# Kernel tuning notes

Hardware: AMD Instinct MI355X
Metric: run time of the kernel (lower is better)

Reference implementation:

```python
import jax, jax.numpy as jnp
import numpy as np

B, S, H, L, NH, DH, FF = 64, 256, 768, 12, 12, 64, 3072
V, MAXP, NTYPE, NI, NS = 30522, 512, 2, 10, 64


def setup_inputs() -> dict:
    key = jax.random.key(0)
    ks = iter(jax.random.split(key, 40))
    n = lambda shp, s=0.02: jax.random.normal(next(ks), shp, jnp.float32) * s
    inp = {
        'input_ids': jax.random.randint(next(ks), (B, S), 0, V),
        'attention_mask': jnp.ones((B, S), jnp.int32),
        'token_type_ids': jnp.zeros((B, S), jnp.int32),
        'intent_labels': jax.random.randint(next(ks), (B,), 0, NI),
        'slot_labels': jax.random.randint(next(ks), (B, S), 0, NS),
        'word_emb': n((V, H)), 'pos_emb': n((MAXP, H)), 'type_emb': n((NTYPE, H)),
        'emb_ln_g': jnp.ones((H,)), 'emb_ln_b': jnp.zeros((H,)),
        'Wq': n((L, H, H)), 'bq': jnp.zeros((L, H)),
        'Wk': n((L, H, H)), 'bk': jnp.zeros((L, H)),
        'Wv': n((L, H, H)), 'bv': jnp.zeros((L, H)),
        'Wo': n((L, H, H)), 'bo': jnp.zeros((L, H)),
        'ln1_g': jnp.ones((L, H)), 'ln1_b': jnp.zeros((L, H)),
        'W1': n((L, H, FF)), 'b1': jnp.zeros((L, FF)),
        'W2': n((L, FF, H)), 'b2': jnp.zeros((L, H)),
        'ln2_g': jnp.ones((L, H)), 'ln2_b': jnp.zeros((L, H)),
        'Wi': n((H, NI)), 'bi': jnp.zeros((NI,)),
        'Ws': n((H, NS)), 'bs': jnp.zeros((NS,)),
        'crf_start': n((NS,), 0.1), 'crf_end': n((NS,), 0.1),
        'crf_trans': n((NS, NS), 0.1),
    }
    return inp


def _ln(x, g, b):
    m = x.mean(-1, keepdims=True)
    v = jnp.square(x - m).mean(-1, keepdims=True)
    return (x - m) * jax.lax.rsqrt(v + 1e-12) * g + b


def _forward(params, input_ids, attention_mask, token_type_ids, intent_labels, slot_labels):
    (word_emb, pos_emb, type_emb, emb_ln_g, emb_ln_b,
     Wq, bq, Wk, bk, Wv, bv, Wo, bo, ln1_g, ln1_b,
     W1, b1, W2, b2, ln2_g, ln2_b,
     Wi, bi, Ws, bs, crf_start, crf_end, crf_trans) = params
    Bn, Sn = input_ids.shape
    Hn = word_emb.shape[1]
    dh = Hn // NH
    # BERT embeddings (dropout is identity in eval)
    x = word_emb[input_ids] + pos_emb[:Sn][None] + type_emb[token_type_ids]
    x = _ln(x, emb_ln_g, emb_ln_b)
    bias = (1.0 - attention_mask.astype(x.dtype))[:, None, None, :] * -1e9  # [B,1,1,S]

    def layer(h, p):
        wq, cq, wk, ck, wv, cv, wo, co, g1, d1, w1, e1, w2, e2, g2, d2 = p
        q = (h @ wq + cq).reshape(Bn, Sn, NH, dh)
        k = (h @ wk + ck).reshape(Bn, Sn, NH, dh)
        v = (h @ wv + cv).reshape(Bn, Sn, NH, dh)
        sc = jnp.einsum('bqnd,bknd->bnqk', q, k) / jnp.sqrt(jnp.float32(dh)) + bias
        a = jax.nn.softmax(sc, axis=-1)
        ctx = jnp.einsum('bnqk,bknd->bqnd', a, v).reshape(Bn, Sn, Hn)
        h2 = _ln(h + ctx @ wo + co, g1, d1)
        ff = jax.nn.gelu(h2 @ w1 + e1, approximate=False)
        return _ln(h2 + ff @ w2 + e2, g2, d2), None

    x, _ = jax.lax.scan(layer, x, (Wq, bq, Wk, bk, Wv, bv, Wo, bo,
                                   ln1_g, ln1_b, W1, b1, W2, b2, ln2_g, ln2_b))
    intent_logits = x[:, 0, :] @ Wi + bi           # [B, NI]
    slot_logits = x @ Ws + bs                      # [B, S, NS]
    # intent cross-entropy (mean over batch)
    lp = jax.nn.log_softmax(intent_logits, axis=-1)
    intent_loss = -jnp.take_along_axis(lp, intent_labels[:, None], axis=1).mean()
    # CRF log-likelihood
    mask = attention_mask.astype(slot_logits.dtype)
    em, tags = slot_logits, slot_labels
    t0 = tags[:, 0]
    score = crf_start[t0] + jnp.take_along_axis(em[:, 0, :], t0[:, None], axis=1)[:, 0]
    prev, cur = tags[:, :-1], tags[:, 1:]
    step_sc = crf_trans[prev, cur] + jnp.take_along_axis(em[:, 1:, :], cur[..., None], axis=2)[..., 0]
    score = score + (step_sc * mask[:, 1:]).sum(1)
    lengths = attention_mask.sum(1)
    last_tag = jnp.take_along_axis(tags, (lengths - 1)[:, None].astype(tags.dtype), axis=1)[:, 0]
    score = score + crf_end[last_tag]
    em_t = jnp.swapaxes(em, 0, 1)    # [S,B,C]
    mk_t = jnp.swapaxes(mask, 0, 1)  # [S,B]
    alpha0 = crf_start[None, :] + em_t[0]

    def crf_step(alpha, xs):
        e, m = xs
        nxt = jax.scipy.special.logsumexp(alpha[:, :, None] + crf_trans[None], axis=1) + e
        return jnp.where(m[:, None] > 0, nxt, alpha), None

    alpha, _ = jax.lax.scan(crf_step, alpha0, (em_t[1:], mk_t[1:]))
    logZ = jax.scipy.special.logsumexp(alpha + crf_end[None, :], axis=1)
    llh = score - logZ                # per-sequence log-likelihood
    crf_loss = -llh.mean()
    return intent_loss + 2.0 * crf_loss


def reference(input_ids, attention_mask, token_type_ids, intent_labels, slot_labels,
              word_emb, pos_emb, type_emb, emb_ln_g, emb_ln_b,
              Wq, bq, Wk, bk, Wv, bv, Wo, bo, ln1_g, ln1_b,
              W1, b1, W2, b2, ln2_g, ln2_b,
              Wi, bi, Ws, bs, crf_start, crf_end, crf_trans):
    params = (word_emb, pos_emb, type_emb, emb_ln_g, emb_ln_b,
              Wq, bq, Wk, bk, Wv, bv, Wo, bo, ln1_g, ln1_b,
              W1, b1, W2, b2, ln2_g, ln2_b,
              Wi, bi, Ws, bs, crf_start, crf_end, crf_trans)
    return _forward(params, input_ids, attention_mask, token_type_ids, intent_labels, slot_labels)
```

## Files before the change

kernel.cpp:

```cpp
#include <hip/hip_runtime.h>
#include <stdint.h>

typedef unsigned short u16;
typedef __attribute__((ext_vector_type(8))) short bh8;
typedef __attribute__((ext_vector_type(4))) float f4;

#define DEV static __device__ __forceinline__

DEV u16 f2bf(float f){ union{float f; uint32_t u;} v; v.f=f; uint32_t r=v.u + 0x7FFFu + ((v.u>>16)&1u); return (u16)(r>>16); }
DEV float bf2f(u16 u){ union{uint32_t u; float f;} v; v.u=((uint32_t)u)<<16; return v.f; }

DEV void mfma16(f4& d, bh8 a, bh8 b){
  d = __builtin_amdgcn_mfma_f32_16x16x32_bf16(a, b, d, 0, 0, 0);
}

DEV float gelu(float v){
  float x = v*0.70710678118f;
  float ax = fabsf(x);
  float tt = 1.0f/(1.0f + 0.3275911f*ax);
  float y = 1.0f - (((((1.061405429f*tt - 1.453152027f)*tt) + 1.421413741f)*tt
                     - 0.284496736f)*tt + 0.254829592f)*tt*__expf(-ax*ax);
  float e = (x<0.f)? -y : y;
  return 0.5f*v*(1.0f+e);
}

#define GLD16(g,l) __builtin_amdgcn_global_load_lds( \
    (__attribute__((address_space(1))) void*)(void*)(g), \
    (__attribute__((address_space(3))) void*)(void*)(l), 16, 0, 0)

struct GemmP { const u16* A; const u16* B; int K; void* C; int ldc;
               const float* b0; const float* b1; const float* b2; const u16* res; };

template<int EPI>
DEV void epi_store(const GemmP& p, int gr, int gc, float v){
  if(EPI==0){
    const float* bp = (gc<768)? p.b0 : (gc<1536? p.b1 : p.b2);
    const int bc = (gc<768)? gc : (gc<1536? gc-768 : gc-1536);
    ((u16*)p.C)[(size_t)gr*p.ldc + gc] = f2bf(v + bp[bc]);
  } else if(EPI==1){
    v += p.b0[gc] + bf2f(p.res[(size_t)gr*p.ldc + gc]);
    ((u16*)p.C)[(size_t)gr*p.ldc + gc] = f2bf(v);
  } else if(EPI==2){
    ((u16*)p.C)[(size_t)gr*p.ldc + gc] = f2bf(gelu(v + p.b0[gc]));
  } else {
    v += (gc<64)? p.b0[gc] : 0.f;
    ((float*)p.C)[(size_t)gr*p.ldc + gc] = v;
  }
}

template<int EPI>
__global__ __launch_bounds__(512)
void gemm256(GemmP p){
  extern __shared__ char smem[];
  const int t=threadIdx.x, l=t&63, w=t>>6;
  const int wr=w>>2, wc=w&3;
  const int m0=blockIdx.x*256, n0=blockIdx.y*256;
  const int K=p.K, NT=K>>6;
  const int fl=l&15, fh=l>>4;

  const int r0=(w*1024+l*16)>>7;
  const int cs=(((l&7)^(l>>3))<<4);
  const char* gA0 = (const char*)p.A + ((size_t)(m0+r0)*K)*2 + cs;
  const char* gB0 = (const char*)p.B + ((size_t)(n0+r0)*K)*2 + cs;
  const size_t rowblk = (size_t)64*K*2;
  char* dA = smem + w*1024;
  char* dB = smem + 32768 + w*1024;

  #define SG_A(T,h,buf) do{ const char* _s=gA0 + (size_t)(T)*128 + (size_t)(h)*2*rowblk; \
    char* _d=dA+(buf)*65536+(h)*16384; GLD16(_s,_d); GLD16(_s+rowblk,_d+8192); }while(0)
  #define SG_B(T,h,buf) do{ const char* _s=gB0 + (size_t)(T)*128 + (size_t)(h)*2*rowblk; \
    char* _d=dB+(buf)*65536+(h)*16384; GLD16(_s,_d); GLD16(_s+rowblk,_d+8192); }while(0)

  int oB[4][2], oA[8][2];
#pragma unroll
  for(int nf=0;nf<4;nf++){ const int rw=wc*64+nf*16+fl;
#pragma unroll
    for(int ks=0;ks<2;ks++) oB[nf][ks] = 32768 + rw*128 + ((ks*64+fh*16) ^ ((rw&7)<<4)); }
#pragma unroll
  for(int mf=0;mf<8;mf++){ const int rw=wr*128+mf*16+fl;
#pragma unroll
    for(int ks=0;ks<2;ks++) oA[mf][ks] = rw*128 + ((ks*64+fh*16) ^ ((rw&7)<<4)); }

  f4 acc[8][4] = {};
  bh8 bfA[4][2], bfB[4][2], afA[2][2], afB[2][2];

  #define MFMA_Q(q, AF, BF) do{ \
    __builtin_amdgcn_s_setprio(1); \
    _Pragma("unroll") \
    for(int j=0;j<2;j++) \
      _Pragma("unroll") \
      for(int nf=0;nf<4;nf++){ mfma16(acc[2*(q)+j][nf], AF[j][0], BF[nf][0]); \
                               mfma16(acc[2*(q)+j][nf], AF[j][1], BF[nf][1]); } \
    __builtin_amdgcn_s_setprio(0); }while(0)

  #define WAIT_LGKM do{ asm volatile("s_waitcnt lgkmcnt(0)":::"memory"); \
    __builtin_amdgcn_sched_barrier(0); }while(0)

  #define TILE(T, CUR, BF) do{ \
    const char* sb = smem + ((CUR)<<16); \
     \
    if((T)+1<NT){ SG_A((T)+1,0,(CUR)^1); SG_A((T)+1,1,(CUR)^1); } \
    _Pragma("unroll") \
    for(int nf=0;nf<4;nf++){ BF[nf][0]=*(const bh8*)(sb+oB[nf][0]); BF[nf][1]=*(const bh8*)(sb+oB[nf][1]); } \
    afA[0][0]=*(const bh8*)(sb+oA[0][0]); afA[0][1]=*(const bh8*)(sb+oA[0][1]); \
    afA[1][0]=*(const bh8*)(sb+oA[1][0]); afA[1][1]=*(const bh8*)(sb+oA[1][1]); \
    __builtin_amdgcn_s_barrier(); WAIT_LGKM; \
    MFMA_Q(0, afA, BF); \
    __builtin_amdgcn_s_barrier(); \
     \
    if((T)+2<NT) SG_B((T)+2,0,(CUR)); \
    afB[0][0]=*(const bh8*)(sb+oA[2][0]); afB[0][1]=*(const bh8*)(sb+oA[2][1]); \
    afB[1][0]=*(const bh8*)(sb+oA[3][0]); afB[1][1]=*(const bh8*)(sb+oA[3][1]); \
    __builtin_amdgcn_s_barrier(); WAIT_LGKM; \
    MFMA_Q(1, afB, BF); \
    __builtin_amdgcn_s_barrier(); \
     \
    if((T)+2<NT) SG_B((T)+2,1,(CUR)); \
    afA[0][0]=*(const bh8*)(sb+oA[4][0]); afA[0][1]=*(const bh8*)(sb+oA[4][1]); \
    afA[1][0]=*(const bh8*)(sb+oA[5][0]); afA[1][1]=*(const bh8*)(sb+oA[5][1]); \
    __builtin_amdgcn_s_barrier(); WAIT_LGKM; \
    MFMA_Q(2, afA, BF); \
    __builtin_amdgcn_s_barrier(); \
     \
    afB[0][0]=*(const bh8*)(sb+oA[6][0]); afB[0][1]=*(const bh8*)(sb+oA[6][1]); \
    afB[1][0]=*(const bh8*)(sb+oA[7][0]); afB[1][1]=*(const bh8*)(sb+oA[7][1]); \
    __builtin_amdgcn_s_barrier(); WAIT_LGKM; \
    MFMA_Q(3, afB, BF); \
    if((T)+2<NT)      asm volatile("s_waitcnt vmcnt(4)":::"memory"); \
    else if((T)+1<NT) asm volatile("s_waitcnt vmcnt(0)":::"memory"); \
    __builtin_amdgcn_s_barrier(); \
  }while(0)

  SG_A(0,0,0); SG_A(0,1,0); SG_B(0,0,0); SG_B(0,1,0);
  if(NT>1){ SG_B(1,0,1); SG_B(1,1,1);
            asm volatile("s_waitcnt vmcnt(4)":::"memory"); }
  else    { asm volatile("s_waitcnt vmcnt(0)":::"memory"); }
  __builtin_amdgcn_s_barrier();

  for(int T=0; T<NT; T+=2){
    TILE(T,   0, bfA);
    TILE(T+1, 1, bfB);
  }
  #undef TILE
  #undef SG_A
  #undef SG_B
  #undef MFMA_Q
  #undef WAIT_LGKM

  const int lr=fh*4;
#pragma unroll
  for(int m=0;m<8;m++)
#pragma unroll
  for(int n=0;n<4;n++)
#pragma unroll
  for(int r=0;r<4;r++){
    epi_store<EPI>(p, m0 + wr*128 + m*16 + lr + r, n0 + wc*64 + n*16 + fl, acc[m][n][r]);
  }
}

template<int EPI>
__global__ __launch_bounds__(256)
void gemm_bt(GemmP p){
  __shared__ __align__(16) u16 As[128*32];
  __shared__ __align__(16) u16 Bs[128*32];
  const int t=threadIdx.x, l=t&63, w=t>>6, wr=w>>1, wc=w&1;
  const int fl=l&15, fh=l>>4;
  const int m0=blockIdx.x*128, n0=blockIdx.y*128;
  const int K=p.K, NT=K>>5;
  const int srow=t>>2;
  const int cs=(((t&3) ^ (srow&3))<<4);
  const char* gA = (const char*)p.A + ((size_t)(m0+srow)*K)*2 + cs;
  const char* gB = (const char*)p.B + ((size_t)(n0+srow)*K)*2 + cs;
  const size_t r64 = (size_t)64*K*2;
  char* dA = (char*)As + t*16;
  char* dB = (char*)Bs + t*16;

  int oA2[4], oB2[4];
#pragma unroll
  for(int mf=0;mf<4;mf++){ const int rw=wr*64+mf*16+fl;
    oA2[mf] = rw*64 + ((fh ^ (rw&3))<<4); }
#pragma unroll
  for(int nf=0;nf<4;nf++){ const int rw=wc*64+nf*16+fl;
    oB2[nf] = rw*64 + ((fh ^ (rw&3))<<4); }

  f4 acc[4][4] = {};
  for(int T=0; T<NT; ++T){
    GLD16(gA + (size_t)T*64, dA);
    GLD16(gA + (size_t)T*64 + r64, dA + 4096);
    GLD16(gB + (size_t)T*64, dB);
    GLD16(gB + (size_t)T*64 + r64, dB + 4096);
    __syncthreads();
    bh8 af[4], bfr[4];
#pragma unroll
    for(int mf=0;mf<4;mf++) af[mf]=*(const bh8*)((const char*)As+oA2[mf]);
#pragma unroll
    for(int nf=0;nf<4;nf++) bfr[nf]=*(const bh8*)((const char*)Bs+oB2[nf]);
#pragma unroll
    for(int m=0;m<4;m++)
#pragma unroll
      for(int n=0;n<4;n++) mfma16(acc[m][n], af[m], bfr[n]);
    __syncthreads();
  }
  const int lr=fh*4;
#pragma unroll
  for(int m=0;m<4;m++)
#pragma unroll
  for(int n=0;n<4;n++)
#pragma unroll
  for(int r=0;r<4;r++){
    epi_store<EPI>(p, m0 + wr*64 + m*16 + lr + r, n0 + wc*64 + n*16 + fl, acc[m][n][r]);
  }
}

__global__ __launch_bounds__(256)
void attn_kernel(const u16* __restrict__ qkv, const int* __restrict__ amask, u16* __restrict__ ctx){
  __shared__ __align__(16) u16 Ks[256*64];
  __shared__ __align__(16) u16 Vt[64*256];
  __shared__ __align__(16) u16 Ps[4*64*64];
  __shared__ float biasS[256];
  const int t=threadIdx.x, l=t&63, w=t>>6;
  const int b=blockIdx.x/12, h=blockIdx.x%12;
  biasS[t] = (1.f - (float)amask[b*256+t]) * -1e9f;
  const u16* kb = qkv + ((size_t)b*256)*2304 + 768 + h*64;
  const u16* vb = kb + 768;
#pragma unroll
  for(int i=0;i<8;i++){
    const int c = t + i*256;
    const int row = c>>3, seg = c&7;
    uint4 kv = *(const uint4*)(kb + (size_t)row*2304 + seg*8);
    const int ba = row*128 + seg*16;
    *(uint4*)((char*)Ks + (ba ^ ((row&7)<<4))) = kv;
    uint4 vv = *(const uint4*)(vb + (size_t)row*2304 + seg*8);
    const u16* pv = (const u16*)&vv;
#pragma unroll
    for(int j=0;j<8;j++){
      const int d = seg*8+j;
      const int bb = d*512 + row*2;
      *(u16*)((char*)Vt + (bb ^ ((d&7)<<4))) = pv[j];
    }
  }
  bh8 aq[4][2];
  const u16* qb = qkv + ((size_t)b*256 + w*64)*2304 + h*64;
#pragma unroll
  for(int m=0;m<4;m++)
#pragma unroll
    for(int ks=0;ks<2;ks++)
      aq[m][ks] = *(const bh8*)(qb + (size_t)(m*16+(l&15))*2304 + ks*32 + (l>>4)*8);
  __syncthreads();
  float mrun[4][4], lrun[4][4];
  f4 o[4][4] = {};
#pragma unroll
  for(int m=0;m<4;m++)
#pragma unroll
    for(int r=0;r<4;r++){ mrun[m][r] = -3e38f; lrun[m][r]=0.f; }
  u16* Pw = Ps + w*4096;
  for(int kt=0;kt<4;kt++){
    f4 sacc[4][4] = {};
#pragma unroll
    for(int ks=0;ks<2;ks++)
#pragma unroll
      for(int n=0;n<4;n++){
        const int row = kt*64 + n*16 + (l&15);
        const int by = row*128 + ks*64 + (l>>4)*16;
        bh8 bk = *(const bh8*)((const char*)Ks + (by ^ ((row&7)<<4)));
#pragma unroll
        for(int m=0;m<4;m++) mfma16(sacc[m][n], aq[m][ks], bk);
      }
#pragma unroll
    for(int m=0;m<4;m++){
      float rmax[4] = {-3e38f,-3e38f,-3e38f,-3e38f};
#pragma unroll
      for(int n=0;n<4;n++){
        const float bi = biasS[kt*64 + n*16 + (l&15)];
#pragma unroll
        for(int r=0;r<4;r++){
          float sv = sacc[m][n][r]*0.125f + bi;
          sacc[m][n][r] = sv;
          rmax[r] = fmaxf(rmax[r], sv);
        }
      }
#pragma unroll
      for(int dd=1; dd<16; dd<<=1)
#pragma unroll
        for(int r=0;r<4;r++) rmax[r] = fmaxf(rmax[r], __shfl_xor(rmax[r], dd));
      float psum[4];
#pragma unroll
      for(int r=0;r<4;r++){
        const float mn = fmaxf(mrun[m][r], rmax[r]);
        const float corr = __expf(mrun[m][r] - mn);
        mrun[m][r] = mn;
        lrun[m][r] *= corr;
#pragma unroll
        for(int nd=0; nd<4; nd++) o[m][nd][r] *= corr;
        psum[r] = 0.f;
      }
#pragma unroll
      for(int n=0;n<4;n++)
#pragma unroll
        for(int r=0;r<4;r++){
          const float pvv = __expf(sacc[m][n][r] - mrun[m][r]);
          sacc[m][n][r] = pvv;
          psum[r] += pvv;
        }
#pragma unroll
      for(int dd=1; dd<16; dd<<=1)
#pragma unroll
        for(int r=0;r<4;r++) psum[r] += __shfl_xor(psum[r], dd);
#pragma unroll
      for(int r=0;r<4;r++) lrun[m][r] += psum[r];
#pragma unroll
      for(int n=0;n<4;n++)
#pragma unroll
        for(int r=0;r<4;r++){
          const int prow = m*16 + (l>>4)*4 + r;
          const int pcol = n*16 + (l&15);
          const int by = prow*128 + pcol*2;
          *(u16*)((char*)Pw + (by ^ ((prow&7)<<4))) = f2bf(sacc[m][n][r]);
        }
    }
#pragma unroll
    for(int ks=0;ks<2;ks++){
      bh8 ap[4];
#pragma unroll
      for(int m=0;m<4;m++){
        const int prow = m*16 + (l&15);
        const int by = prow*128 + (ks*32 + (l>>4)*8)*2;
        ap[m] = *(const bh8*)((const char*)Pw + (by ^ ((prow&7)<<4)));
      }
#pragma unroll
      for(int nd=0; nd<4; nd++){
        const int dR = nd*16 + (l&15);
        const int by = dR*512 + (kt*64 + ks*32 + (l>>4)*8)*2;
        bh8 bv = *(const bh8*)((const char*)Vt + (by ^ ((dR&7)<<4)));
#pragma unroll
        for(int m=0;m<4;m++) mfma16(o[m][nd], ap[m], bv);
      }
    }
  }
#pragma unroll
  for(int m=0;m<4;m++)
#pragma unroll
  for(int nd=0; nd<4; nd++)
#pragma unroll
  for(int r=0;r<4;r++){
    const int row = w*64 + m*16 + (l>>4)*4 + r;
    const float vv = o[m][nd][r] / lrun[m][r];
    ctx[((size_t)b*256 + row)*768 + h*64 + nd*16 + (l&15)] = f2bf(vv);
  }
}

__global__ void ln_kernel(const u16* __restrict__ in, const float* __restrict__ g,
                          const float* __restrict__ b, u16* __restrict__ out){
  const int row = blockIdx.x, t = threadIdx.x;
  __shared__ float red[8];
  const u16* rp = in + (size_t)row*768;
  float v[3]; float s=0.f, q=0.f;
#pragma unroll
  for(int i=0;i<3;i++){ float x = bf2f(rp[t + i*256]); v[i]=x; s+=x; q+=x*x; }
#pragma unroll
  for(int dd=1; dd<64; dd<<=1){ s += __shfl_xor(s,dd); q += __shfl_xor(q,dd); }
  if((t&63)==0){ red[t>>6]=s; red[4+(t>>6)]=q; }
  __syncthreads();
  s = red[0]+red[1]+red[2]+red[3];
  q = red[4]+red[5]+red[6]+red[7];
  const float mean = s*(1.f/768.f);
  float var = q*(1.f/768.f) - mean*mean; var = fmaxf(var, 0.f);
  const float rs = rsqrtf(var + 1e-12f);
  u16* op = out + (size_t)row*768;
#pragma unroll
  for(int i=0;i<3;i++){ const int hh=t+i*256; op[hh] = f2bf((v[i]-mean)*rs*g[hh] + b[hh]); }
}

__global__ void embed_ln(const int* __restrict__ ids, const int* __restrict__ tti,
    const float* __restrict__ we, const float* __restrict__ pe, const float* __restrict__ te,
    const float* __restrict__ g, const float* __restrict__ bb, u16* __restrict__ x){
  const int tok = blockIdx.x, t = threadIdx.x;
  __shared__ float red[8];
  const int id = ids[tok], tyid = tti[tok], s0 = tok & 255;
  float v[3]; float s=0.f,q=0.f;
#pragma unroll
  for(int i=0;i<3;i++){
    const int hh = t+i*256;
    float x0 = we[(size_t)id*768+hh] + pe[(size_t)s0*768+hh] + te[(size_t)tyid*768+hh];
    v[i]=x0; s+=x0; q+=x0*x0;
  }
#pragma unroll
  for(int dd=1; dd<64; dd<<=1){ s += __shfl_xor(s,dd); q += __shfl_xor(q,dd); }
  if((t&63)==0){ red[t>>6]=s; red[4+(t>>6)]=q; }
  __syncthreads();
  s = red[0]+red[1]+red[2]+red[3];
  q = red[4]+red[5]+red[6]+red[7];
  const float mean = s*(1.f/768.f);
  float var = q*(1.f/768.f) - mean*mean; var = fmaxf(var, 0.f);
  const float rs = rsqrtf(var + 1e-12f);
#pragma unroll
  for(int i=0;i<3;i++){ const int hh=t+i*256; x[(size_t)tok*768+hh] = f2bf((v[i]-mean)*rs*g[hh] + bb[hh]); }
}

__global__ void transpose_cvt(const float* __restrict__ src, u16* __restrict__ dst, int R, int C){
  __shared__ float sm[32][33];
  const int ntc = C>>5;
  const int tr = blockIdx.x/ntc, tc = blockIdx.x - tr*ntc;
  const int r0 = tr<<5, c0 = tc<<5;
  const int tx = threadIdx.x, ty2 = threadIdx.y;
#pragma unroll
  for(int i=0;i<4;i++) sm[ty2+i*8][tx] = src[(size_t)(r0+ty2+i*8)*C + c0+tx];
  __syncthreads();
#pragma unroll
  for(int i=0;i<4;i++) dst[(size_t)(c0+ty2+i*8)*R + r0+tx] = f2bf(sm[tx][ty2+i*8]);
}

__global__ void conv_layer(const float* __restrict__ Wq, const float* __restrict__ Wk,
    const float* __restrict__ Wv, const float* __restrict__ Wo,
    const float* __restrict__ W1, const float* __restrict__ W2, u16* __restrict__ Wt){
  __shared__ float sm[32][33];
  const int bid = blockIdx.x;
  const float* src; u16* dst; int R, C, tt;
  if(bid<2304){
    R=768; C=768; const int mi = bid/576; tt = bid - mi*576;
    src = (mi==0?Wq: mi==1?Wk: mi==2?Wv: Wo);
    dst = Wt + (size_t)mi*589824;
  } else if(bid<4608){ R=768; C=3072; tt=bid-2304; src=W1; dst=Wt+2359296; }
  else { R=3072; C=768; tt=bid-4608; src=W2; dst=Wt+4718592; }
  const int ntc=C>>5; const int tr=tt/ntc, tc=tt-tr*ntc;
  const int r0=tr<<5, c0=tc<<5, tx=threadIdx.x, ty2=threadIdx.y;
#pragma unroll
  for(int i=0;i<4;i++) sm[ty2+i*8][tx] = src[(size_t)(r0+ty2+i*8)*C + c0+tx];
  __syncthreads();
#pragma unroll
  for(int i=0;i<4;i++) dst[(size_t)(c0+ty2+i*8)*R + r0+tx] = f2bf(sm[tx][ty2+i*8]);
}

__global__ void intent_kernel(const u16* __restrict__ x, const float* __restrict__ Wi,
    const float* __restrict__ bi, const int* __restrict__ lab, float* __restrict__ parts){
  const int b = blockIdx.x, t = threadIdx.x;
  __shared__ float xs[768];
  __shared__ float lg[10];
  const u16* rp = x + ((size_t)b*256)*768;
#pragma unroll
  for(int i=0;i<3;i++) xs[t+i*256] = bf2f(rp[t+i*256]);
  __syncthreads();
  if(t<10){
    float s = bi[t];
    for(int k=0;k<768;k++) s += xs[k]*Wi[(size_t)k*10 + t];
    lg[t] = s;
  }
  __syncthreads();
  if(t==0){
    float m = lg[0];
    for(int j=1;j<10;j++) m = fmaxf(m, lg[j]);
    float se = 0.f;
    for(int j=0;j<10;j++) se += expf(lg[j]-m);
    parts[b] = (logf(se) + m) - lg[lab[b]];
  }
}

__global__ __launch_bounds__(64)
void crf_kernel(const float* __restrict__ em, const int* __restrict__ tags,
    const int* __restrict__ amask, const float* __restrict__ cs, const float* __restrict__ ce,
    const float* __restrict__ tr, float* __restrict__ parts){
  const int b = blockIdx.x, j = threadIdx.x;
  const float* eb = em + (size_t)b*256*128;
  const int* tg = tags + b*256;
  const int* mk = amask + b*256;
  __shared__ __align__(16) float aS[64];
  float Etr[64];
#pragma unroll
  for(int i=0;i<64;i++) Etr[i] = __expf(tr[i*64 + j]);
  float sc = 0.f; int len = 0;
  for(int s=j+1; s<256; s+=64){
    const int pv = tg[s-1], cu = tg[s];
    sc += (tr[pv*64+cu] + eb[(size_t)s*128+cu]) * (float)mk[s];
  }
  for(int s=j; s<256; s+=64) len += mk[s];
#pragma unroll
  for(int dd=1; dd<64; dd<<=1){ sc += __shfl_xor(sc,dd); len += __shfl_xor(len,dd); }
  const int t0 = tg[0];
  float score = sc + cs[t0] + eb[t0] + ce[tg[len-1]];
  float a = __expf(cs[j] + eb[j]);
  float logc = 0.f;
  float em_s = eb[128 + j];
  int   mk_s = mk[1];
  for(int s=1; s<256; s++){
    const int sn = (s<255)? s+1 : s;
    const float em_n = eb[(size_t)sn*128 + j];
    const int   mk_n = mk[sn];
    aS[j] = a;
    __syncthreads();
    float acc0=0.f, acc1=0.f, acc2=0.f, acc3=0.f;
    const float4* ap = (const float4*)aS;
#pragma unroll
    for(int q2=0;q2<16;q2++){
      const float4 av = ap[q2];
      acc0 += av.x*Etr[4*q2+0];
      acc1 += av.y*Etr[4*q2+1];
      acc2 += av.z*Etr[4*q2+2];
      acc3 += av.w*Etr[4*q2+3];
    }
    __syncthreads();
    const float nxt = ((acc0+acc1)+(acc2+acc3)) * __expf(em_s);
    a = (mk_s > 0) ? nxt : a;
    if((s&7)==7){
      const float c = __shfl(a, 0);
      logc += __logf(c);
      a *= (1.f/c);
    }
    em_s = em_n; mk_s = mk_n;
  }
  float v2 = logf(a) + logc + ce[j];
  float am2 = v2;
#pragma unroll
  for(int dd=1; dd<64; dd<<=1) am2 = fmaxf(am2, __shfl_xor(am2,dd));
  float se = __expf(v2 - am2);
#pragma unroll
  for(int dd=1; dd<64; dd<<=1) se += __shfl_xor(se,dd);
  if(j==0) parts[64+b] = (logf(se)+am2) - score;
}

__global__ void final_reduce(const float* __restrict__ parts, float* __restrict__ out){
  const int t = threadIdx.x;
  float a = parts[t], c = parts[64+t];
#pragma unroll
  for(int dd=1; dd<64; dd<<=1){ a += __shfl_xor(a,dd); c += __shfl_xor(c,dd); }
  if(t==0) out[0] = a*(1.f/64.f) + 2.f*c*(1.f/64.f);
}

extern "C" void kernel_launch(void* const* d_in, const int* in_sizes, int n_in,
                              void* d_out, int out_size, void* d_ws, size_t ws_size,
                              hipStream_t stream){
  (void)in_sizes; (void)n_in; (void)out_size;
  const int* ids   = (const int*)d_in[0];
  const int* amask = (const int*)d_in[1];
  const int* tti   = (const int*)d_in[2];
  const int* ilab  = (const int*)d_in[3];
  const int* slab  = (const int*)d_in[4];
  const float* we  = (const float*)d_in[5];
  const float* pe  = (const float*)d_in[6];
  const float* te  = (const float*)d_in[7];
  const float* eg  = (const float*)d_in[8];
  const float* ebt = (const float*)d_in[9];
  const float* Wq  = (const float*)d_in[10];
  const float* bq  = (const float*)d_in[11];
  const float* Wk  = (const float*)d_in[12];
  const float* bkk = (const float*)d_in[13];
  const float* Wv  = (const float*)d_in[14];
  const float* bvv = (const float*)d_in[15];
  const float* Wo  = (const float*)d_in[16];
  const float* bo  = (const float*)d_in[17];
  const float* l1g = (const float*)d_in[18];
  const float* l1b = (const float*)d_in[19];
  const float* W1  = (const float*)d_in[20];
  const float* b1  = (const float*)d_in[21];
  const float* W2  = (const float*)d_in[22];
  const float* b2  = (const float*)d_in[23];
  const float* l2g = (const float*)d_in[24];
  const float* l2b = (const float*)d_in[25];
  const float* Wi  = (const float*)d_in[26];
  const float* bi  = (const float*)d_in[27];
  const float* Wsp = (const float*)d_in[28];
  const float* bs  = (const float*)d_in[29];
  const float* cs  = (const float*)d_in[30];
  const float* ce  = (const float*)d_in[31];
  const float* ctr = (const float*)d_in[32];

  char* ws = (char*)d_ws;
  size_t off = 0;
  auto alloc = [&](size_t bytes)->void*{ void* p = ws + off; off += (bytes+255)&~(size_t)255; return p; };
  u16* x     = (u16*)alloc(16384ull*768*2);
  u16* h2    = (u16*)alloc(16384ull*768*2);
  u16* y     = (u16*)alloc(16384ull*768*2);
  u16* qkv   = (u16*)alloc(16384ull*2304*2);
  u16* cf    = (u16*)alloc(16384ull*3072*2);
  u16* Wt    = (u16*)alloc(7077888ull*2);
  u16* WsT   = (u16*)alloc(128ull*768*2);
  float* slots = (float*)alloc(16384ull*128*4);
  float* parts = (float*)alloc(512);
  if(off > ws_size) return;

  (void)hipFuncSetAttribute((const void*)gemm256<0>, hipFuncAttributeMaxDynamicSharedMemorySize, 131072);
  (void)hipFuncSetAttribute((const void*)gemm256<1>, hipFuncAttributeMaxDynamicSharedMemorySize, 131072);
  (void)hipFuncSetAttribute((const void*)gemm256<2>, hipFuncAttributeMaxDynamicSharedMemorySize, 131072);

  dim3 T256(256), T512(512), T328(32,8);
  embed_ln<<<dim3(16384), T256, 0, stream>>>(ids, tti, we, pe, te, eg, ebt, x);
  transpose_cvt<<<dim3(48), T328, 0, stream>>>(Wsp, WsT, 768, 64);
  for(int L=0; L<12; L++){
    const size_t oH = (size_t)L*768*768, oF = (size_t)L*768*3072;
    conv_layer<<<dim3(6912), T328, 0, stream>>>(Wq+oH, Wk+oH, Wv+oH, Wo+oH, W1+oF, W2+oF, Wt);
    GemmP pq{ x, Wt, 768, qkv, 2304, bq+L*768, bkk+L*768, bvv+L*768, nullptr };
    gemm256<0><<<dim3(64,9), T512, 131072, stream>>>(pq);
    attn_kernel<<<dim3(768), T256, 0, stream>>>(qkv, amask, cf);
    GemmP po{ cf, Wt+1769472, 768, y, 768, bo+L*768, nullptr, nullptr, x };
    gemm256<1><<<dim3(64,3), T512, 131072, stream>>>(po);
    ln_kernel<<<dim3(16384), T256, 0, stream>>>(y, l1g+L*768, l1b+L*768, h2);
    GemmP p1{ h2, Wt+2359296, 768, cf, 3072, b1+L*3072, nullptr, nullptr, nullptr };
    gemm256<2><<<dim3(64,12), T512, 131072, stream>>>(p1);
    GemmP p2{ cf, Wt+4718592, 3072, y, 768, b2+L*768, nullptr, nullptr, h2 };
    gemm256<1><<<dim3(64,3), T512, 131072, stream>>>(p2);
    ln_kernel<<<dim3(16384), T256, 0, stream>>>(y, l2g+L*768, l2b+L*768, x);
  }
  GemmP psl{ x, WsT, 768, slots, 128, bs, nullptr, nullptr, nullptr };
  gemm_bt<3><<<dim3(128,1), T256, 0, stream>>>(psl);
  intent_kernel<<<dim3(64), T256, 0, stream>>>(x, Wi, bi, ilab, parts);
  crf_kernel<<<dim3(64), dim3(64), 0, stream>>>(slots, slab, amask, cs, ce, ctr, parts);
  final_reduce<<<dim3(1), dim3(64), 0, stream>>>(parts, (float*)d_out);
}
```

Measured before the change: 5.506 ms.

## Use 128x128 GEMM tiles for narrow projections and vectorize layernorm kernels

```diff
diff --git a/kernel.cpp b/kernel.cpp
--- a/kernel.cpp
+++ b/kernel.cpp
@@ -4,6 +4,7 @@
 typedef unsigned short u16;
 typedef __attribute__((ext_vector_type(8))) short bh8;
 typedef __attribute__((ext_vector_type(4))) float f4;
+typedef __attribute__((ext_vector_type(4))) short s4v;
 
 #define DEV static __device__ __forceinline__
 
@@ -41,10 +42,56 @@
     v += p.b0[gc] + bf2f(p.res[(size_t)gr*p.ldc + gc]);
     ((u16*)p.C)[(size_t)gr*p.ldc + gc] = f2bf(v);
   } else if(EPI==2){
-    ((u16*)p.C)[(size_t)gr*p.ldc + gc] = f2bf(gelu(v + p.b0[gc]));
+    __builtin_nontemporal_store(f2bf(gelu(v + p.b0[gc])), &((u16*)p.C)[(size_t)gr*p.ldc + gc]);
   } else {
     v += (gc<64)? p.b0[gc] : 0.f;
     ((float*)p.C)[(size_t)gr*p.ldc + gc] = v;
+  }
+}
+
+template<int EPI>
+__global__ __launch_bounds__(256,4)
+void gemm128(GemmP p){
+  __shared__ __align__(16) u16 As[128*32];
+  __shared__ __align__(16) u16 Bs[128*32];
+  const int t=threadIdx.x, l=t&63, w=t>>6, wr=w>>1, wc=w&1;
+  const int m0=blockIdx.x*128, n0=blockIdx.y*128;
+  const int K=p.K, NT=K>>5;
+  const int srow = t>>2;
+  const int cs = (((t&3) ^ ((t>>3)&3))<<4);
+  const u16* Ab = p.A + (size_t)(m0+srow)*K;
+  const u16* Bb = p.B + (size_t)(n0+srow)*K;
+
+  f4 acc[4][4] = {};
+  for(int T=0; T<NT; ++T){
+    const char* a0 = (const char*)(Ab + T*32) + cs;
+    const char* b0 = (const char*)(Bb + T*32) + cs;
+    GLD16(a0,                    (char*)As + t*16);
+    GLD16(a0 + (size_t)64*K*2,   (char*)As + t*16 + 4096);
+    GLD16(b0,                    (char*)Bs + t*16);
+    GLD16(b0 + (size_t)64*K*2,   (char*)Bs + t*16 + 4096);
+    __syncthreads();
+    bh8 af[4], bfr[4];
+#pragma unroll
+    for(int mf=0;mf<4;mf++){ const int rw=wr*64+mf*16+(l&15);
+      af[mf]=*(const bh8*)((const char*)As + rw*64 + (((l>>4) ^ ((rw>>1)&3))<<4)); }
+#pragma unroll
+    for(int nf=0;nf<4;nf++){ const int rw=wc*64+nf*16+(l&15);
+      bfr[nf]=*(const bh8*)((const char*)Bs + rw*64 + (((l>>4) ^ ((rw>>1)&3))<<4)); }
+#pragma unroll
+    for(int m=0;m<4;m++)
+#pragma unroll
+      for(int n=0;n<4;n++) mfma16(acc[m][n], af[m], bfr[n]);
+    __syncthreads();
+  }
+  const int lr=(l>>4)*4, lc=l&15;
+#pragma unroll
+  for(int m=0;m<4;m++)
+#pragma unroll
+  for(int n=0;n<4;n++)
+#pragma unroll
+  for(int r=0;r<4;r++){
+    epi_store<EPI>(p, m0 + wr*64 + m*16 + lr + r, n0 + wc*64 + n*16 + lc, acc[m][n][r]);
   }
 }
 
@@ -98,7 +145,6 @@
 
   #define TILE(T, CUR, BF) do{ \
     const char* sb = smem + ((CUR)<<16); \
-     \
     if((T)+1<NT){ SG_A((T)+1,0,(CUR)^1); SG_A((T)+1,1,(CUR)^1); } \
     _Pragma("unroll") \
     for(int nf=0;nf<4;nf++){ BF[nf][0]=*(const bh8*)(sb+oB[nf][0]); BF[nf][1]=*(const bh8*)(sb+oB[nf][1]); } \
@@ -107,21 +153,18 @@
     __builtin_amdgcn_s_barrier(); WAIT_LGKM; \
     MFMA_Q(0, afA, BF); \
     __builtin_amdgcn_s_barrier(); \
-     \
     if((T)+2<NT) SG_B((T)+2,0,(CUR)); \
     afB[0][0]=*(const bh8*)(sb+oA[2][0]); afB[0][1]=*(const bh8*)(sb+oA[2][1]); \
     afB[1][0]=*(const bh8*)(sb+oA[3][0]); afB[1][1]=*(const bh8*)(sb+oA[3][1]); \
     __builtin_amdgcn_s_barrier(); WAIT_LGKM; \
     MFMA_Q(1, afB, BF); \
     __builtin_amdgcn_s_barrier(); \
-     \
     if((T)+2<NT) SG_B((T)+2,1,(CUR)); \
     afA[0][0]=*(const bh8*)(sb+oA[4][0]); afA[0][1]=*(const bh8*)(sb+oA[4][1]); \
     afA[1][0]=*(const bh8*)(sb+oA[5][0]); afA[1][1]=*(const bh8*)(sb+oA[5][1]); \
     __builtin_amdgcn_s_barrier(); WAIT_LGKM; \
     MFMA_Q(2, afA, BF); \
     __builtin_amdgcn_s_barrier(); \
-     \
     afB[0][0]=*(const bh8*)(sb+oA[6][0]); afB[0][1]=*(const bh8*)(sb+oA[6][1]); \
     afB[1][0]=*(const bh8*)(sb+oA[7][0]); afB[1][1]=*(const bh8*)(sb+oA[7][1]); \
     __builtin_amdgcn_s_barrier(); WAIT_LGKM; \
@@ -155,60 +198,6 @@
 #pragma unroll
   for(int r=0;r<4;r++){
     epi_store<EPI>(p, m0 + wr*128 + m*16 + lr + r, n0 + wc*64 + n*16 + fl, acc[m][n][r]);
-  }
-}
-
-template<int EPI>
-__global__ __launch_bounds__(256)
-void gemm_bt(GemmP p){
-  __shared__ __align__(16) u16 As[128*32];
-  __shared__ __align__(16) u16 Bs[128*32];
-  const int t=threadIdx.x, l=t&63, w=t>>6, wr=w>>1, wc=w&1;
-  const int fl=l&15, fh=l>>4;
-  const int m0=blockIdx.x*128, n0=blockIdx.y*128;
-  const int K=p.K, NT=K>>5;
-  const int srow=t>>2;
-  const int cs=(((t&3) ^ (srow&3))<<4);
-  const char* gA = (const char*)p.A + ((size_t)(m0+srow)*K)*2 + cs;
-  const char* gB = (const char*)p.B + ((size_t)(n0+srow)*K)*2 + cs;
-  const size_t r64 = (size_t)64*K*2;
-  char* dA = (char*)As + t*16;
-  char* dB = (char*)Bs + t*16;
-
-  int oA2[4], oB2[4];
-#pragma unroll
-  for(int mf=0;mf<4;mf++){ const int rw=wr*64+mf*16+fl;
-    oA2[mf] = rw*64 + ((fh ^ (rw&3))<<4); }
-#pragma unroll
-  for(int nf=0;nf<4;nf++){ const int rw=wc*64+nf*16+fl;
-    oB2[nf] = rw*64 + ((fh ^ (rw&3))<<4); }
-
-  f4 acc[4][4] = {};
-  for(int T=0; T<NT; ++T){
-    GLD16(gA + (size_t)T*64, dA);
-    GLD16(gA + (size_t)T*64 + r64, dA + 4096);
-    GLD16(gB + (size_t)T*64, dB);
-    GLD16(gB + (size_t)T*64 + r64, dB + 4096);
-    __syncthreads();
-    bh8 af[4], bfr[4];
-#pragma unroll
-    for(int mf=0;mf<4;mf++) af[mf]=*(const bh8*)((const char*)As+oA2[mf]);
-#pragma unroll
-    for(int nf=0;nf<4;nf++) bfr[nf]=*(const bh8*)((const char*)Bs+oB2[nf]);
-#pragma unroll
-    for(int m=0;m<4;m++)
-#pragma unroll
-      for(int n=0;n<4;n++) mfma16(acc[m][n], af[m], bfr[n]);
-    __syncthreads();
-  }
-  const int lr=fh*4;
-#pragma unroll
-  for(int m=0;m<4;m++)
-#pragma unroll
-  for(int n=0;n<4;n++)
-#pragma unroll
-  for(int r=0;r<4;r++){
-    epi_store<EPI>(p, m0 + wr*64 + m*16 + lr + r, n0 + wc*64 + n*16 + fl, acc[m][n][r]);
   }
 }
 
@@ -353,22 +342,33 @@
                           const float* __restrict__ b, u16* __restrict__ out){
   const int row = blockIdx.x, t = threadIdx.x;
   __shared__ float red[8];
-  const u16* rp = in + (size_t)row*768;
-  float v[3]; float s=0.f, q=0.f;
-#pragma unroll
-  for(int i=0;i<3;i++){ float x = bf2f(rp[t + i*256]); v[i]=x; s+=x; q+=x*x; }
+  const bool act = t < 192;
+  float v0=0,v1=0,v2=0,v3=0;
+  if(act){
+    s4v x = *(const s4v*)(in + (size_t)row*768 + t*4);
+    v0=bf2f((u16)x[0]); v1=bf2f((u16)x[1]); v2=bf2f((u16)x[2]); v3=bf2f((u16)x[3]);
+  }
+  float s = (v0+v1)+(v2+v3);
+  float q = (v0*v0+v1*v1)+(v2*v2+v3*v3);
 #pragma unroll
   for(int dd=1; dd<64; dd<<=1){ s += __shfl_xor(s,dd); q += __shfl_xor(q,dd); }
   if((t&63)==0){ red[t>>6]=s; red[4+(t>>6)]=q; }
   __syncthreads();
-  s = red[0]+red[1]+red[2]+red[3];
-  q = red[4]+red[5]+red[6]+red[7];
+  s = red[0]+red[1]+red[2];
+  q = red[4]+red[5]+red[6];
   const float mean = s*(1.f/768.f);
   float var = q*(1.f/768.f) - mean*mean; var = fmaxf(var, 0.f);
   const float rs = rsqrtf(var + 1e-12f);
-  u16* op = out + (size_t)row*768;
-#pragma unroll
-  for(int i=0;i<3;i++){ const int hh=t+i*256; op[hh] = f2bf((v[i]-mean)*rs*g[hh] + b[hh]); }
+  if(act){
+    float4 gv = *(const float4*)(g + t*4);
+    float4 bv = *(const float4*)(b + t*4);
+    s4v o;
+    o[0]=(short)f2bf((v0-mean)*rs*gv.x + bv.x);
+    o[1]=(short)f2bf((v1-mean)*rs*gv.y + bv.y);
+    o[2]=(short)f2bf((v2-mean)*rs*gv.z + bv.z);
+    o[3]=(short)f2bf((v3-mean)*rs*gv.w + bv.w);
+    *(s4v*)(out + (size_t)row*768 + t*4) = o;
+  }
 }
 
 __global__ void embed_ln(const int* __restrict__ ids, const int* __restrict__ tti,
@@ -377,24 +377,35 @@
   const int tok = blockIdx.x, t = threadIdx.x;
   __shared__ float red[8];
   const int id = ids[tok], tyid = tti[tok], s0 = tok & 255;
-  float v[3]; float s=0.f,q=0.f;
-#pragma unroll
-  for(int i=0;i<3;i++){
-    const int hh = t+i*256;
-    float x0 = we[(size_t)id*768+hh] + pe[(size_t)s0*768+hh] + te[(size_t)tyid*768+hh];
-    v[i]=x0; s+=x0; q+=x0*x0;
-  }
+  const bool act = t < 192;
+  float v0=0,v1=0,v2=0,v3=0;
+  if(act){
+    float4 a = *(const float4*)(we + (size_t)id*768 + t*4);
+    float4 pp = *(const float4*)(pe + (size_t)s0*768 + t*4);
+    float4 ty = *(const float4*)(te + (size_t)tyid*768 + t*4);
+    v0=a.x+pp.x+ty.x; v1=a.y+pp.y+ty.y; v2=a.z+pp.z+ty.z; v3=a.w+pp.w+ty.w;
+  }
+  float s = (v0+v1)+(v2+v3);
+  float q = (v0*v0+v1*v1)+(v2*v2+v3*v3);
 #pragma unroll
   for(int dd=1; dd<64; dd<<=1){ s += __shfl_xor(s,dd); q += __shfl_xor(q,dd); }
   if((t&63)==0){ red[t>>6]=s; red[4+(t>>6)]=q; }
   __syncthreads();
-  s = red[0]+red[1]+red[2]+red[3];
-  q = red[4]+red[5]+red[6]+red[7];
+  s = red[0]+red[1]+red[2];
+  q = red[4]+red[5]+red[6];
   const float mean = s*(1.f/768.f);
   float var = q*(1.f/768.f) - mean*mean; var = fmaxf(var, 0.f);
   const float rs = rsqrtf(var + 1e-12f);
-#pragma unroll
-  for(int i=0;i<3;i++){ const int hh=t+i*256; x[(size_t)tok*768+hh] = f2bf((v[i]-mean)*rs*g[hh] + bb[hh]); }
+  if(act){
+    float4 gv = *(const float4*)(g + t*4);
+    float4 bv = *(const float4*)(bb + t*4);
+    s4v o;
+    o[0]=(short)f2bf((v0-mean)*rs*gv.x + bv.x);
+    o[1]=(short)f2bf((v1-mean)*rs*gv.y + bv.y);
+    o[2]=(short)f2bf((v2-mean)*rs*gv.z + bv.z);
+    o[3]=(short)f2bf((v3-mean)*rs*gv.w + bv.w);
+    *(s4v*)(x + (size_t)tok*768 + t*4) = o;
+  }
 }
 
 __global__ void transpose_cvt(const float* __restrict__ src, u16* __restrict__ dst, int R, int C){
@@ -577,8 +588,6 @@
   float* parts = (float*)alloc(512);
   if(off > ws_size) return;
 
-  (void)hipFuncSetAttribute((const void*)gemm256<0>, hipFuncAttributeMaxDynamicSharedMemorySize, 131072);
-  (void)hipFuncSetAttribute((const void*)gemm256<1>, hipFuncAttributeMaxDynamicSharedMemorySize, 131072);
   (void)hipFuncSetAttribute((const void*)gemm256<2>, hipFuncAttributeMaxDynamicSharedMemorySize, 131072);
 
   dim3 T256(256), T512(512), T328(32,8);
@@ -588,19 +597,19 @@
     const size_t oH = (size_t)L*768*768, oF = (size_t)L*768*3072;
     conv_layer<<<dim3(6912), T328, 0, stream>>>(Wq+oH, Wk+oH, Wv+oH, Wo+oH, W1+oF, W2+oF, Wt);
     GemmP pq{ x, Wt, 768, qkv, 2304, bq+L*768, bkk+L*768, bvv+L*768, nullptr };
-    gemm256<0><<<dim3(64,9), T512, 131072, stream>>>(pq);
+    gemm128<0><<<dim3(128,18), T256, 0, stream>>>(pq);
     attn_kernel<<<dim3(768), T256, 0, stream>>>(qkv, amask, cf);
     GemmP po{ cf, Wt+1769472, 768, y, 768, bo+L*768, nullptr, nullptr, x };
-    gemm256<1><<<dim3(64,3), T512, 131072, stream>>>(po);
+    gemm128<1><<<dim3(128,6), T256, 0, stream>>>(po);
     ln_kernel<<<dim3(16384), T256, 0, stream>>>(y, l1g+L*768, l1b+L*768, h2);
     GemmP p1{ h2, Wt+2359296, 768, cf, 3072, b1+L*3072, nullptr, nullptr, nullptr };
     gemm256<2><<<dim3(64,12), T512, 131072, stream>>>(p1);
     GemmP p2{ cf, Wt+4718592, 3072, y, 768, b2+L*768, nullptr, nullptr, h2 };
-    gemm256<1><<<dim3(64,3), T512, 131072, stream>>>(p2);
+    gemm128<1><<<dim3(128,6), T256, 0, stream>>>(p2);
     ln_kernel<<<dim3(16384), T256, 0, stream>>>(y, l2g+L*768, l2b+L*768, x);
   }
   GemmP psl{ x, WsT, 768, slots, 128, bs, nullptr, nullptr, nullptr };
-  gemm_bt<3><<<dim3(128,1), T256, 0, stream>>>(psl);
+  gemm128<3><<<dim3(128,1), T256, 0, stream>>>(psl);
   intent_kernel<<<dim3(64), T256, 0, stream>>>(x, Wi, bi, ilab, parts);
   crf_kernel<<<dim3(64), dim3(64), 0, stream>>>(slots, slab, amask, cs, ce, ctr, parts);
   final_reduce<<<dim3(1), dim3(64), 0, stream>>>(parts, (float*)d_out);
```

Result: slower. 5.749 ms (+4.4%).
